# Optimization experiments

Hardware: AMD Instinct MI355X
Metric: run time of the kernel (lower is better)

The kernel has to match this reference:

```python
import jax, jax.numpy as jnp
import numpy as np

N_NODES = 100000
N_EDGES = 1600000
D_IN, D_EMB, D_POOL = 256, 128, 64
EPS = 1e-6


def setup_inputs() -> dict:
    key = jax.random.key(0)
    ks = jax.random.split(key, 10)
    x = jax.random.normal(ks[0], (N_NODES, D_IN), dtype=jnp.float32)
    edge_src = jax.random.randint(ks[1], (N_EDGES,), 0, N_NODES, dtype=jnp.int32)
    edge_dst = jax.random.randint(ks[2], (N_EDGES,), 0, N_NODES, dtype=jnp.int32)
    edge_weight = jax.random.uniform(ks[3], (N_EDGES,), dtype=jnp.float32)
    # glorot-ish init for the three GraphConvolution weights
    w1 = jax.random.normal(ks[4], (D_IN, D_EMB), dtype=jnp.float32) / np.sqrt(D_IN)
    b1 = jnp.zeros((D_EMB,), dtype=jnp.float32)
    wp = jax.random.normal(ks[5], (D_EMB, D_POOL), dtype=jnp.float32) / np.sqrt(D_EMB)
    bp = jnp.zeros((D_POOL,), dtype=jnp.float32)
    w2 = jax.random.normal(ks[6], (D_EMB, D_POOL), dtype=jnp.float32) / np.sqrt(D_EMB)
    b2 = jnp.zeros((D_POOL,), dtype=jnp.float32)
    return {"x": x, "edge_src": edge_src, "edge_dst": edge_dst,
            "edge_weight": edge_weight, "w1": w1, "b1": b1,
            "wp": wp, "bp": bp, "w2": w2, "b2": b2}


def _gcn(h, w, b, edge_src, edge_dst, edge_weight, n_nodes):
    # GraphConvolution: support = h @ w ; out = adj @ support + b (sparse spmm)
    support = h @ w                                  # [N, d_out]
    msgs = edge_weight[:, None] * support[edge_src]  # [E, d_out] gather
    agg = jax.ops.segment_sum(msgs, edge_dst, num_segments=n_nodes)
    return agg + b


def _pairnorm_si(h):
    # PairNorm mode 'PN-SI' (scale=1): center over nodes, row-wise L2 normalize
    h = h - jnp.mean(h, axis=0, keepdims=True)
    rownorm = jnp.sqrt(EPS + jnp.sum(h * h, axis=1, keepdims=True))
    return h / rownorm


def reference(x, edge_src, edge_dst, edge_weight, w1, b1, wp, bp, w2, b2):
    n = x.shape[0]
    enc1 = _gcn(x, w1, b1, edge_src, edge_dst, edge_weight, n)
    enc1 = jax.nn.relu(_pairnorm_si(enc1))
    pool1 = _gcn(enc1, wp, bp, edge_src, edge_dst, edge_weight, n)
    pool1 = jax.nn.softmax(_pairnorm_si(pool1), axis=-1)
    enc2 = _gcn(enc1, w2, b2, edge_src, edge_dst, edge_weight, n)
    enc2 = jax.nn.relu(_pairnorm_si(enc2))
    return enc2, pool1
```

## Files before the change

kernel.cpp:

```cpp
#include <hip/hip_runtime.h>
#include <stdint.h>

#define N_NODES 100000
#define N_EDGES 1600000
#define CAP 48

typedef __attribute__((ext_vector_type(8))) short bf16x8;
typedef __attribute__((ext_vector_type(4))) float f32x4;

__device__ __forceinline__ uint32_t f2bf(float f) {
  uint32_t u = __float_as_uint(f);
  u += 0x7fffu + ((u >> 16) & 1);
  return u >> 16;
}
__device__ __forceinline__ float bf_lo(uint32_t v) { return __uint_as_float(v << 16); }
__device__ __forceinline__ float bf_hi(uint32_t v) { return __uint_as_float(v & 0xffff0000u); }
__device__ __forceinline__ uint32_t pack2(float a, float b) { return f2bf(a) | (f2bf(b) << 16); }

__global__ void k_pack(const float* __restrict__ w1, const float* __restrict__ wp,
                       const float* __restrict__ w2, uint16_t* __restrict__ wT1,
                       uint16_t* __restrict__ wTc) {
  int i = blockIdx.x * 256 + threadIdx.x;
  if (i < 128 * 256) {
    int n = i >> 8, k = i & 255;
    wT1[n * 256 + (k ^ ((n & 7) << 3))] = (uint16_t)f2bf(w1[k * 128 + n]);
  }
  int j = i - 128 * 256;
  if (j >= 0 && j < 128 * 128) {
    int n = j >> 7, k = j & 127;
    wTc[n * 128 + (k ^ ((n & 7) << 3))] =
        (uint16_t)f2bf((n < 64) ? wp[k * 64 + n] : w2[k * 64 + (n - 64)]);
  }
}

__global__ __launch_bounds__(512) void k_g1s(const float* __restrict__ A,
                                             const uint16_t* __restrict__ wTs,
                                             uint16_t* __restrict__ C, int M,
                                             const int* __restrict__ esrc,
                                             const int* __restrict__ edst,
                                             const float* __restrict__ ew,
                                             int* __restrict__ fill,
                                             int2* __restrict__ rec) {
  __shared__ uint16_t bs[128 * 256];
  {
    const float4* s = (const float4*)wTs;
    float4* d = (float4*)bs;
#pragma unroll
    for (int i = 0; i < 8; i++) d[i * 512 + threadIdx.x] = s[i * 512 + threadIdx.x];
  }
  __syncthreads();

  int wave = threadIdx.x >> 6, lane = threadIdx.x & 63;
  if (wave >= 4) {
    int S = gridDim.x * 256;
    int sid = (blockIdx.x * 4 + (wave - 4)) * 64 + lane;
    for (int e = sid; e < N_EDGES; e += S) {
      int d = edst[e];
      int pos = atomicAdd(&fill[d], 1);
      rec[(size_t)d * CAP + pos] = make_int2(esrc[e], __float_as_int(ew[e]));
    }
    return;
  }

  int m0 = (blockIdx.x * 4 + wave) * 16;
  int quad = lane >> 4, mcol = lane & 15;
  int xsw = (mcol & 7) << 3;
  int arow = m0 + mcol;
  bool av = arow < M;

  float4 abuf[16];
  const float* ap = A + (size_t)arow * 256 + quad * 8;
  if (av) {
#pragma unroll
    for (int t = 0; t < 8; t++) {
      abuf[2 * t]     = *(const float4*)(ap + t * 32);
      abuf[2 * t + 1] = *(const float4*)(ap + t * 32 + 4);
    }
  } else {
#pragma unroll
    for (int t = 0; t < 16; t++) abuf[t] = (float4){0.f, 0.f, 0.f, 0.f};
  }

  const uint16_t* bp = bs + mcol * 256;

  f32x4 acc[8];
#pragma unroll
  for (int nt = 0; nt < 8; nt++) acc[nt] = (f32x4){0.f, 0.f, 0.f, 0.f};

#pragma unroll
  for (int it = 0; it < 8; it++) {
    float4 lo = abuf[2 * it], hi = abuf[2 * it + 1];
    bf16x8 a;
    a[0] = (short)f2bf(lo.x); a[1] = (short)f2bf(lo.y);
    a[2] = (short)f2bf(lo.z); a[3] = (short)f2bf(lo.w);
    a[4] = (short)f2bf(hi.x); a[5] = (short)f2bf(hi.y);
    a[6] = (short)f2bf(hi.z); a[7] = (short)f2bf(hi.w);
#pragma unroll
    for (int nt = 0; nt < 8; nt++) {
      bf16x8 b = *(const bf16x8*)(bp + nt * 4096 + ((it * 32 + quad * 8) ^ xsw));
      acc[nt] = __builtin_amdgcn_mfma_f32_16x16x32_bf16(a, b, acc[nt], 0, 0, 0);
    }
  }
#pragma unroll
  for (int r = 0; r < 4; r++) {
    int row = m0 + quad * 4 + r;
    if (row < M) {
#pragma unroll
      for (int nt = 0; nt < 8; nt++)
        C[(size_t)row * 128 + nt * 16 + mcol] = (uint16_t)f2bf(acc[nt][r]);
    }
  }
}

__global__ __launch_bounds__(256) void k_gemm2(const uint16_t* __restrict__ A,
                                               const uint16_t* __restrict__ wTs,
                                               uint16_t* __restrict__ C,
                                               const float* __restrict__ cs, int M) {
  __shared__ uint16_t bs[128 * 128];
  __shared__ float csn[128];
  {
    const float4* s = (const float4*)wTs;
    float4* d = (float4*)bs;
#pragma unroll
    for (int i = 0; i < 8; i++) d[i * 256 + threadIdx.x] = s[i * 256 + threadIdx.x];
    if (threadIdx.x < 128) csn[threadIdx.x] = cs[threadIdx.x] * (1.0f / (float)N_NODES);
  }
  __syncthreads();

  int wave = threadIdx.x >> 6, lane = threadIdx.x & 63;
  int m0 = (blockIdx.x * 4 + wave) * 16;
  int quad = lane >> 4, mcol = lane & 15;
  int xsw = (mcol & 7) << 3;
  int arow = m0 + mcol;
  bool av = arow < M;

  bf16x8 abuf[4];
  const uint16_t* ap = A + (size_t)arow * 128 + quad * 8;
  if (av) {
#pragma unroll
    for (int t = 0; t < 4; t++) abuf[t] = *(const bf16x8*)(ap + t * 32);
  } else {
#pragma unroll
    for (int t = 0; t < 4; t++) abuf[t] = (bf16x8){};
  }

  float hf[4][8];
  float ssq = 0.f;
#pragma unroll
  for (int t = 0; t < 4; t++) {
#pragma unroll
    for (int j = 0; j < 8; j++) {
      float h = av ? (__uint_as_float(((uint32_t)(uint16_t)abuf[t][j]) << 16)
                      - csn[quad * 8 + t * 32 + j])
                   : 0.f;
      hf[t][j] = h;
      ssq += h * h;
    }
  }
  ssq += __shfl_xor(ssq, 16, 64);
  ssq += __shfl_xor(ssq, 32, 64);
  float rinv = rsqrtf(1e-6f + ssq);
  bf16x8 afr[4];
#pragma unroll
  for (int t = 0; t < 4; t++)
#pragma unroll
    for (int j = 0; j < 8; j++)
      afr[t][j] = (short)f2bf(fmaxf(hf[t][j] * rinv, 0.f));

  const uint16_t* bp = bs + mcol * 128;

  f32x4 acc[8];
#pragma unroll
  for (int nt = 0; nt < 8; nt++) acc[nt] = (f32x4){0.f, 0.f, 0.f, 0.f};

#pragma unroll
  for (int it = 0; it < 4; it++) {
#pragma unroll
    for (int nt = 0; nt < 8; nt++) {
      bf16x8 b = *(const bf16x8*)(bp + nt * 2048 + ((it * 32 + quad * 8) ^ xsw));
      acc[nt] = __builtin_amdgcn_mfma_f32_16x16x32_bf16(afr[it], b, acc[nt], 0, 0, 0);
    }
  }
#pragma unroll
  for (int r = 0; r < 4; r++) {
    int row = m0 + quad * 4 + r;
    if (row < M) {
#pragma unroll
      for (int nt = 0; nt < 8; nt++)
        C[(size_t)row * 128 + nt * 16 + mcol] = (uint16_t)f2bf(acc[nt][r]);
    }
  }
}

__global__ __launch_bounds__(256) void k_spmm(const uint16_t* __restrict__ sup,
                                              const int* __restrict__ fill,
                                              const int2* __restrict__ rec,
                                              uint16_t* __restrict__ agg,
                                              float* __restrict__ cs) {
  int wave = threadIdx.x >> 6, lane = threadIdx.x & 63;
  int rbase = blockIdx.x * 64 + wave * 16;
  float c0acc = 0.f, c1acc = 0.f;

  for (int pr = 0; pr < 8; ++pr) {
    int r0 = rbase + pr * 2;
    if (r0 >= N_NODES) break;
    int r1 = r0 + 1;
    int c0 = fill[r0], c1 = fill[r1];
    const int2* p0 = rec + (size_t)r0 * CAP;
    const int2* p1 = rec + (size_t)r1 * CAP;
    float a00 = 0.f, a01 = 0.f, a10 = 0.f, a11 = 0.f;
    int n = c0 > c1 ? c0 : c1;
    for (int k = 0; k < n; k += 8) {
      int2 ra[8], rb[8];
      uint32_t va[8], vb[8];
      bool q0 = k < c0, q1 = k < c1;
      if (q0) {
#pragma unroll
        for (int u = 0; u < 8; u++) ra[u] = p0[k + u];
      }
      if (q1) {
#pragma unroll
        for (int u = 0; u < 8; u++) rb[u] = p1[k + u];
      }
      float wa[8], wb[8];
#pragma unroll
      for (int u = 0; u < 8; u++) {
        bool ok = q0 && (k + u < c0);
        int sidx = ok ? ra[u].x : 0;
        wa[u] = ok ? __int_as_float(ra[u].y) : 0.f;
        va[u] = *(const uint32_t*)(sup + (size_t)sidx * 128 + lane * 2);
      }
#pragma unroll
      for (int u = 0; u < 8; u++) {
        bool ok = q1 && (k + u < c1);
        int sidx = ok ? rb[u].x : 0;
        wb[u] = ok ? __int_as_float(rb[u].y) : 0.f;
        vb[u] = *(const uint32_t*)(sup + (size_t)sidx * 128 + lane * 2);
      }
#pragma unroll
      for (int u = 0; u < 8; u++) {
        a00 += wa[u] * bf_lo(va[u]);
        a01 += wa[u] * bf_hi(va[u]);
        a10 += wb[u] * bf_lo(vb[u]);
        a11 += wb[u] * bf_hi(vb[u]);
      }
    }
    *(uint32_t*)(agg + (size_t)r0 * 128 + lane * 2) = pack2(a00, a01);
    *(uint32_t*)(agg + (size_t)r1 * 128 + lane * 2) = pack2(a10, a11);
    c0acc += a00 + a10;
    c1acc += a01 + a11;
  }

  __shared__ float sd[4][128];
  sd[wave][lane * 2]     = c0acc;
  sd[wave][lane * 2 + 1] = c1acc;
  __syncthreads();
  if (threadIdx.x < 128) {
    float s = sd[0][threadIdx.x] + sd[1][threadIdx.x] +
              sd[2][threadIdx.x] + sd[3][threadIdx.x];
    atomicAdd(&cs[threadIdx.x], s);
  }
}

__global__ __launch_bounds__(256) void k_final(const uint16_t* __restrict__ agg,
                                               const float* __restrict__ cs,
                                               float* __restrict__ out) {
  int row = blockIdx.x * 4 + (threadIdx.x >> 6);
  if (row >= N_NODES) return;
  int lane = threadIdx.x & 63;
  const float invn = 1.0f / (float)N_NODES;
  uint32_t v = *(const uint32_t*)(agg + (size_t)row * 128 + lane * 2);
  float h0 = bf_lo(v) - cs[lane * 2] * invn;
  float h1 = bf_hi(v) - cs[lane * 2 + 1] * invn;
  float ss = h0 * h0 + h1 * h1;
#pragma unroll
  for (int m = 1; m < 32; m <<= 1) ss += __shfl_xor(ss, m, 64);
  float rinv = rsqrtf(1e-6f + ss);
  float p0 = h0 * rinv, p1 = h1 * rinv;
  if (lane < 32) {
    float mx = fmaxf(p0, p1);
#pragma unroll
    for (int m = 1; m < 32; m <<= 1) mx = fmaxf(mx, __shfl_xor(mx, m, 64));
    float e0 = __expf(p0 - mx), e1 = __expf(p1 - mx);
    float sum = e0 + e1;
#pragma unroll
    for (int m = 1; m < 32; m <<= 1) sum += __shfl_xor(sum, m, 64);
    float inv = 1.0f / sum;
    float2 o = {e0 * inv, e1 * inv};
    *(float2*)(out + (size_t)N_NODES * 64 + (size_t)row * 64 + lane * 2) = o;
  } else {
    int l = lane - 32;
    float2 o = {fmaxf(p0, 0.f), fmaxf(p1, 0.f)};
    *(float2*)(out + (size_t)row * 64 + l * 2) = o;
  }
}

extern "C" void kernel_launch(void* const* d_in, const int* in_sizes, int n_in,
                              void* d_out, int out_size, void* d_ws, size_t ws_size,
                              hipStream_t stream) {
  const float* x    = (const float*)d_in[0];
  const int*   esrc = (const int*)d_in[1];
  const int*   edst = (const int*)d_in[2];
  const float* ew   = (const float*)d_in[3];
  const float* w1   = (const float*)d_in[4];
  const float* wp   = (const float*)d_in[6];
  const float* w2   = (const float*)d_in[8];
  float* out = (float*)d_out;

  char* ws = (char*)d_ws;
  size_t off = 0;
  auto alloc = [&](size_t bytes) {
    char* p = ws + off;
    off += (bytes + 255) & ~(size_t)255;
    return p;
  };
  uint16_t* support = (uint16_t*)alloc((size_t)N_NODES * 128 * 2);
  uint16_t* agg     = (uint16_t*)alloc((size_t)N_NODES * 128 * 2);
  int2*     rec     = (int2*)alloc((size_t)N_NODES * CAP * 8);
  size_t zero_start = off;
  int*      fill    = (int*)alloc((size_t)N_NODES * 4);
  float*    cs      = (float*)alloc(256 * 4);
  size_t zero_bytes = off - zero_start;
  uint16_t* wT1     = (uint16_t*)alloc(128 * 256 * 2);
  uint16_t* wTc     = (uint16_t*)alloc(128 * 128 * 2);
  (void)ws_size; (void)in_sizes; (void)n_in; (void)out_size;

  hipMemsetAsync(fill, 0, zero_bytes, stream);

  k_pack<<<192, 256, 0, stream>>>(w1, wp, w2, wT1, wTc);

  k_g1s<<<(N_NODES + 63) / 64, 512, 0, stream>>>(x, wT1, support, N_NODES,
                                                 esrc, edst, ew, fill, rec);
  k_spmm<<<(N_NODES + 63) / 64, 256, 0, stream>>>(support, fill, rec, agg, cs);

  k_gemm2<<<(N_NODES + 63) / 64, 256, 0, stream>>>(agg, wTc, support, cs, N_NODES);
  k_spmm<<<(N_NODES + 63) / 64, 256, 0, stream>>>(support, fill, rec, agg, cs + 128);
  k_final<<<(N_NODES + 3) / 4, 256, 0, stream>>>(agg, cs + 128, out);
}
```

Measured before the change: 523.4 us.

## Split spmm into one row pair per wave and replicate column-sum atomics

The spmm kernel now gives each wave a single pair of rows instead of looping over eight pairs, which raises the grid size eightfold and exposes more latency-hiding parallelism for the gather. To offset the larger number of blocks doing atomic adds on the column sums, the sums are spread across 8 replicated buffers chosen by block index. The gemm2 and final kernels sum the replicas when they read them. The cost is more atomics and per-block reduction overhead, plus a few extra loads in the consumers.

```diff
diff --git a/kernel.cpp b/kernel.cpp
--- a/kernel.cpp
+++ b/kernel.cpp
@@ -4,6 +4,7 @@
 #define N_NODES 100000
 #define N_EDGES 1600000
 #define CAP 48
+#define NREP 8
 
 typedef __attribute__((ext_vector_type(8))) short bf16x8;
 typedef __attribute__((ext_vector_type(4))) float f32x4;
@@ -115,7 +116,7 @@
 __global__ __launch_bounds__(256) void k_gemm2(const uint16_t* __restrict__ A,
                                                const uint16_t* __restrict__ wTs,
                                                uint16_t* __restrict__ C,
-                                               const float* __restrict__ cs, int M) {
+                                               const float* __restrict__ csrep, int M) {
   __shared__ uint16_t bs[128 * 128];
   __shared__ float csn[128];
   {
@@ -123,7 +124,12 @@
     float4* d = (float4*)bs;
 #pragma unroll
     for (int i = 0; i < 8; i++) d[i * 256 + threadIdx.x] = s[i * 256 + threadIdx.x];
-    if (threadIdx.x < 128) csn[threadIdx.x] = cs[threadIdx.x] * (1.0f / (float)N_NODES);
+    if (threadIdx.x < 128) {
+      float s0 = 0.f;
+#pragma unroll
+      for (int r = 0; r < NREP; r++) s0 += csrep[r * 128 + threadIdx.x];
+      csn[threadIdx.x] = s0 * (1.0f / (float)N_NODES);
+    }
   }
   __syncthreads();
 
@@ -196,19 +202,15 @@
                                               const int* __restrict__ fill,
                                               const int2* __restrict__ rec,
                                               uint16_t* __restrict__ agg,
-                                              float* __restrict__ cs) {
+                                              float* __restrict__ csrep) {
   int wave = threadIdx.x >> 6, lane = threadIdx.x & 63;
-  int rbase = blockIdx.x * 64 + wave * 16;
-  float c0acc = 0.f, c1acc = 0.f;
-
-  for (int pr = 0; pr < 8; ++pr) {
-    int r0 = rbase + pr * 2;
-    if (r0 >= N_NODES) break;
+  int r0 = (blockIdx.x * 4 + wave) * 2;
+  float a00 = 0.f, a01 = 0.f, a10 = 0.f, a11 = 0.f;
+  if (r0 < N_NODES) {
     int r1 = r0 + 1;
     int c0 = fill[r0], c1 = fill[r1];
     const int2* p0 = rec + (size_t)r0 * CAP;
     const int2* p1 = rec + (size_t)r1 * CAP;
-    float a00 = 0.f, a01 = 0.f, a10 = 0.f, a11 = 0.f;
     int n = c0 > c1 ? c0 : c1;
     for (int k = 0; k < n; k += 8) {
       int2 ra[8], rb[8];
@@ -247,31 +249,35 @@
     }
     *(uint32_t*)(agg + (size_t)r0 * 128 + lane * 2) = pack2(a00, a01);
     *(uint32_t*)(agg + (size_t)r1 * 128 + lane * 2) = pack2(a10, a11);
-    c0acc += a00 + a10;
-    c1acc += a01 + a11;
   }
 
   __shared__ float sd[4][128];
-  sd[wave][lane * 2]     = c0acc;
-  sd[wave][lane * 2 + 1] = c1acc;
+  sd[wave][lane * 2]     = a00 + a10;
+  sd[wave][lane * 2 + 1] = a01 + a11;
   __syncthreads();
   if (threadIdx.x < 128) {
     float s = sd[0][threadIdx.x] + sd[1][threadIdx.x] +
               sd[2][threadIdx.x] + sd[3][threadIdx.x];
-    atomicAdd(&cs[threadIdx.x], s);
+    atomicAdd(&csrep[(blockIdx.x & (NREP - 1)) * 128 + threadIdx.x], s);
   }
 }
 
 __global__ __launch_bounds__(256) void k_final(const uint16_t* __restrict__ agg,
-                                               const float* __restrict__ cs,
+                                               const float* __restrict__ csrep,
                                                float* __restrict__ out) {
   int row = blockIdx.x * 4 + (threadIdx.x >> 6);
   if (row >= N_NODES) return;
   int lane = threadIdx.x & 63;
   const float invn = 1.0f / (float)N_NODES;
+  float cs0 = 0.f, cs1 = 0.f;
+#pragma unroll
+  for (int r = 0; r < NREP; r++) {
+    cs0 += csrep[r * 128 + lane * 2];
+    cs1 += csrep[r * 128 + lane * 2 + 1];
+  }
   uint32_t v = *(const uint32_t*)(agg + (size_t)row * 128 + lane * 2);
-  float h0 = bf_lo(v) - cs[lane * 2] * invn;
-  float h1 = bf_hi(v) - cs[lane * 2 + 1] * invn;
+  float h0 = bf_lo(v) - cs0 * invn;
+  float h1 = bf_hi(v) - cs1 * invn;
   float ss = h0 * h0 + h1 * h1;
 #pragma unroll
   for (int m = 1; m < 32; m <<= 1) ss += __shfl_xor(ss, m, 64);
@@ -319,7 +325,7 @@
   int2*     rec     = (int2*)alloc((size_t)N_NODES * CAP * 8);
   size_t zero_start = off;
   int*      fill    = (int*)alloc((size_t)N_NODES * 4);
-  float*    cs      = (float*)alloc(256 * 4);
+  float*    cs      = (float*)alloc(2 * NREP * 128 * 4);
   size_t zero_bytes = off - zero_start;
   uint16_t* wT1     = (uint16_t*)alloc(128 * 256 * 2);
   uint16_t* wTc     = (uint16_t*)alloc(128 * 128 * 2);
@@ -331,9 +337,9 @@
 
   k_g1s<<<(N_NODES + 63) / 64, 512, 0, stream>>>(x, wT1, support, N_NODES,
                                                  esrc, edst, ew, fill, rec);
-  k_spmm<<<(N_NODES + 63) / 64, 256, 0, stream>>>(support, fill, rec, agg, cs);
+  k_spmm<<<(N_NODES + 7) / 8, 256, 0, stream>>>(support, fill, rec, agg, cs);
 
   k_gemm2<<<(N_NODES + 63) / 64, 256, 0, stream>>>(agg, wTc, support, cs, N_NODES);
-  k_spmm<<<(N_NODES + 63) / 64, 256, 0, stream>>>(support, fill, rec, agg, cs + 128);
-  k_final<<<(N_NODES + 3) / 4, 256, 0, stream>>>(agg, cs + 128, out);
-}
+  k_spmm<<<(N_NODES + 7) / 8, 256, 0, stream>>>(support, fill, rec, agg, cs + NREP * 128);
+  k_final<<<(N_NODES + 3) / 4, 256, 0, stream>>>(agg, cs + NREP * 128, out);
+}
```

Result: slower. 676.5 us (+29.3%).
